# Optimization experiments

Measured on AMD Instinct MI355X. Metric: run time of the kernel, lower is better.

## Reference

```python
import jax, jax.numpy as jnp
import numpy as np

B, N, D_IN, D_OUT = 8, 2048, 256, 256
BN_EPS = 1e-5
SELU_ALPHA = 1.6732632423543772
SELU_SCALE = 1.0507009873554805


def setup_inputs() -> dict:
    key = jax.random.key(0)
    k1, k2, k3, k4 = jax.random.split(key, 4)
    lim_lin = 1.0 / np.sqrt(D_IN)
    return {
        "x": jax.random.normal(k1, (B, N, D_IN), dtype=jnp.float32),
        "w_map": jax.random.uniform(k2, (D_IN,), jnp.float32, -lim_lin, lim_lin),
        "w_att": jax.random.uniform(k3, (D_OUT, D_IN), jnp.float32, -lim_lin, lim_lin),
        "w_res": jax.random.uniform(k4, (D_OUT, D_IN), jnp.float32, -lim_lin, lim_lin),
        "gamma": jnp.ones((D_OUT,), jnp.float32),
        "beta": jnp.zeros((D_OUT,), jnp.float32),
    }


def _selu(x):
    x_clamped = jnp.clip(x, -10.0, 10.0)
    return SELU_SCALE * jnp.where(x > 0, x, SELU_ALPHA * (jnp.exp(x_clamped) - 1.0))


def reference(x, w_map, w_att, w_res, gamma, beta):
    # scores[b,i,j] = sum_d w_map[d] * x[b,i,d] * x[b,j,d]  (== W_map(x_i*x_j))
    scores = jnp.einsum("bid,bjd->bij", x * w_map, x)  # [B,N,N]
    attn = jax.nn.softmax(scores, axis=-1)
    aggregated = jnp.einsum("bij,bjd->bid", attn, x)  # [B,N,D]
    out = aggregated @ w_att.T + x @ w_res.T  # [B,N,D_OUT]
    # BatchNorm1d in training mode: stats over (batch, nodes) per channel, biased var
    mean = jnp.mean(out, axis=(0, 1))
    var = jnp.mean(jnp.square(out - mean), axis=(0, 1))
    out = (out - mean) * jax.lax.rsqrt(var + BN_EPS) * gamma + beta
    return _selu(out)
```

## Files before the change

### kernel.cpp

```cpp
#include <hip/hip_runtime.h>
#include <hip/hip_bf16.h>


typedef __attribute__((ext_vector_type(8)))  short bf16x8;
typedef __attribute__((ext_vector_type(4)))  float f32x4;
typedef __attribute__((ext_vector_type(16))) float f32x16;

#define MFMA16(a, b, c) __builtin_amdgcn_mfma_f32_16x16x32_bf16((a), (b), (c), 0, 0, 0)
#define MFMA32(a, b, c) __builtin_amdgcn_mfma_f32_32x32x16_bf16((a), (b), (c), 0, 0, 0)

constexpr int   NB = 8, NN = 2048;
constexpr int   ROWS = NB * NN;
constexpr float BN_EPS = 1e-5f;
constexpr float SELU_ALPHA = 1.6732632423543772f;
constexpr float SELU_SCALE = 1.0507009873554805f;

__device__ __forceinline__ unsigned short f2bf(float f) {
  union { float f; unsigned int u; } v; v.f = f;
  unsigned int u = v.u;
  u += 0x7FFFu + ((u >> 16) & 1u);
  return (unsigned short)(u >> 16);
}
__device__ __forceinline__ float bf2f(unsigned short h) {
  union { float f; unsigned int u; } v; v.u = ((unsigned int)h) << 16;
  return v.f;
}
__device__ __forceinline__ unsigned int pk2(float lo, float hi) {
  return (unsigned int)f2bf(lo) | ((unsigned int)f2bf(hi) << 16);
}

__device__ __forceinline__ void async_copy16(const unsigned short* g, unsigned short* l) {
  __builtin_amdgcn_global_load_lds(
      (const __attribute__((address_space(1))) void*)g,
      (__attribute__((address_space(3))) void*)l, 16, 0, 0);
}

__global__ __launch_bounds__(256) void k0_prep(const float* __restrict__ x,
                                               unsigned short* __restrict__ XR,
                                               unsigned short* __restrict__ Xt,
                                               const float* __restrict__ w_att,
                                               const float* __restrict__ w_res,
                                               unsigned short* __restrict__ WC,
                                               float* __restrict__ sums) {
  __shared__ unsigned short Ls[32 * 264];
  const int t = threadIdx.x;
  const int b = blockIdx.x & 7, rt = blockIdx.x >> 3;
  const int grb = b * NN + rt * 32;
  const int c = (t & 31) * 8, r0 = t >> 5;
#pragma unroll
  for (int q = 0; q < 4; ++q) {
    int r = r0 + q * 8;
    const float* xp = x + (size_t)(grb + r) * 256 + c;
    float4 a = *(const float4*)xp;
    float4 d = *(const float4*)(xp + 4);
    union { unsigned short s[8]; uint4 v; } xb;
    xb.s[0] = f2bf(a.x); xb.s[1] = f2bf(a.y); xb.s[2] = f2bf(a.z); xb.s[3] = f2bf(a.w);
    xb.s[4] = f2bf(d.x); xb.s[5] = f2bf(d.y); xb.s[6] = f2bf(d.z); xb.s[7] = f2bf(d.w);
    *(uint4*)(XR + (size_t)(grb + r) * 256 + c) = xb.v;
    *(uint4*)&Ls[r * 264 + c] = xb.v;
  }
  __syncthreads();
  unsigned short* dstB = Xt + (size_t)b * 256 * 2048 + rt * 32;
  const int dl = t >> 2, jc = t & 3;
#pragma unroll
  for (int pass = 0; pass < 4; ++pass) {
    int d = pass * 64 + dl;
    union { unsigned short s[8]; uint4 v; } o;
#pragma unroll
    for (int j = 0; j < 8; ++j) o.s[j] = Ls[(jc * 8 + j) * 264 + d];
    *(uint4*)(dstB + (size_t)d * 2048 + jc * 8) = o.v;
  }
  if (blockIdx.x == 0 && t < 256) ((float4*)sums)[t] = make_float4(0.f, 0.f, 0.f, 0.f);
  if (blockIdx.x < 64) {
    int f = (blockIdx.x * 256 + t) * 8;
    int cc = f >> 9, k = f & 511;
    const float* src = (k < 256) ? (w_att + cc * 256 + k) : (w_res + cc * 256 + (k - 256));
    float4 a = *(const float4*)src;
    float4 d = *(const float4*)(src + 4);
    union { unsigned short s[8]; uint4 v; } o;
    o.s[0] = f2bf(a.x); o.s[1] = f2bf(a.y); o.s[2] = f2bf(a.z); o.s[3] = f2bf(a.w);
    o.s[4] = f2bf(d.x); o.s[5] = f2bf(d.y); o.s[6] = f2bf(d.z); o.s[7] = f2bf(d.w);
    *(uint4*)(WC + f) = o.v;
  }
}

__global__ __launch_bounds__(512, 2) void k1_attn(const float* __restrict__ w_map,
                                                  const unsigned short* __restrict__ XR,
                                                  const unsigned short* __restrict__ Xt,
                                                  unsigned short* __restrict__ Opart,
                                                  float* __restrict__ Lpart) {
  __shared__ unsigned short Ks[2][32 * 256];
  __shared__ unsigned short Vt[2][256 * 32];

  const int t = threadIdx.x;
  const int w = t >> 6, lane = t & 63;
  const int l31 = lane & 31, h = lane >> 5;
  const int qb = blockIdx.x >> 2, p = blockIdx.x & 3;
  const int b = qb >> 3;
  const int rowbase = qb * 256;
  const int jb0 = b * 2048 + p * 512;
  const unsigned short* Xtb = Xt + (size_t)b * 256 * 2048;

  int kSrc[2], vSrc[2];
#pragma unroll
  for (int q = 0; q < 2; ++q) {
    int cch = q * 512 + t;
    int kj = cch >> 5, kck = cch & 31;
    int pj = ((kj >> 3) & 1) * 16 + ((kj >> 4) & 1) * 4 + (kj & 3) + ((kj >> 2) & 1) * 8;
    kSrc[q] = (jb0 + pj) * 256 + ((kck ^ (kj & 7)) * 8);
    int vd = cch >> 2, vcj = cch & 3;
    vSrc[q] = vd * 2048 + p * 512 + ((vcj ^ ((vd >> 1) & 3)) * 8);
  }

#pragma unroll
  for (int q = 0; q < 2; ++q)
    async_copy16(XR + kSrc[q], &Ks[0][(q * 512 + t) * 8]);
#pragma unroll
  for (int q = 0; q < 2; ++q)
    async_copy16(Xtb + vSrc[q], &Vt[0][(q * 512 + t) * 8]);

  bf16x8 qf[16];
  {
    const unsigned short* xrow = XR + (size_t)(rowbase + w * 32 + l31) * 256 + h * 8;
#pragma unroll
    for (int kc = 0; kc < 16; ++kc) {
      bf16x8 xb = *(const bf16x8*)(xrow + kc * 16);
      const float* wp = w_map + kc * 16 + h * 8;
      float4 w0 = *(const float4*)wp, w1 = *(const float4*)(wp + 4);
      float wv[8] = {w0.x, w0.y, w0.z, w0.w, w1.x, w1.y, w1.z, w1.w};
      bf16x8 qv;
#pragma unroll
      for (int i = 0; i < 8; ++i)
        qv[i] = (short)f2bf(bf2f((unsigned short)xb[i]) * wv[i]);
      qf[kc] = qv;
    }
  }

  const f32x16 fz16 = {0.f,0.f,0.f,0.f, 0.f,0.f,0.f,0.f, 0.f,0.f,0.f,0.f, 0.f,0.f,0.f,0.f};
  f32x16 oacc[8];
#pragma unroll
  for (int i = 0; i < 8; ++i) oacc[i] = fz16;
  float rsum = 0.f;

  const int sw7 = l31 & 7;
  const int vkey = (l31 >> 1) & 3;

  for (int jt = 0; jt < 16; ++jt) {
    const int cur = jt & 1;
    __syncthreads();
    if (jt < 15) {
#pragma unroll
      for (int q = 0; q < 2; ++q)
        async_copy16(XR + kSrc[q] + (jt + 1) * 8192, &Ks[cur ^ 1][(q * 512 + t) * 8]);
#pragma unroll
      for (int q = 0; q < 2; ++q)
        async_copy16(Xtb + vSrc[q] + (jt + 1) * 32, &Vt[cur ^ 1][(q * 512 + t) * 8]);
    }
    f32x16 sA = fz16, sB = fz16;
#pragma unroll
    for (int kc = 0; kc < 8; ++kc) {
      bf16x8 kf = *(const bf16x8*)&Ks[cur][l31 * 256 + (((2 * kc + h) ^ sw7) * 8)];
      sA = MFMA32(kf, qf[kc], sA);
    }
#pragma unroll
    for (int kc = 8; kc < 16; ++kc) {
      bf16x8 kf = *(const bf16x8*)&Ks[cur][l31 * 256 + (((2 * kc + h) ^ sw7) * 8)];
      sB = MFMA32(kf, qf[kc], sB);
    }
    float pv[16];
#pragma unroll
    for (int r = 0; r < 16; ++r) {
      pv[r] = __expf(sA[r] + sB[r]);
      rsum += pv[r];
    }
    union { unsigned int u[4]; bf16x8 v; } a0, a1;
    a0.u[0] = pk2(pv[0],  pv[1]);
    a0.u[1] = pk2(pv[2],  pv[3]);
    a0.u[2] = pk2(pv[8],  pv[9]);
    a0.u[3] = pk2(pv[10], pv[11]);
    a1.u[0] = pk2(pv[4],  pv[5]);
    a1.u[1] = pk2(pv[6],  pv[7]);
    a1.u[2] = pk2(pv[12], pv[13]);
    a1.u[3] = pk2(pv[14], pv[15]);
#pragma unroll
    for (int dt = 0; dt < 8; ++dt) {
      const int dbase = (dt * 32 + l31) * 32;
      bf16x8 v0 = *(const bf16x8*)&Vt[cur][dbase + ((h ^ vkey) * 8)];
      oacc[dt] = MFMA32(a0.v, v0, oacc[dt]);
      bf16x8 v1 = *(const bf16x8*)&Vt[cur][dbase + (((2 + h) ^ vkey) * 8)];
      oacc[dt] = MFMA32(a1.v, v1, oacc[dt]);
    }
  }

  float rsT = rsum + __shfl_xor(rsum, 32);
  if (h == 0) Lpart[(size_t)p * ROWS + rowbase + w * 32 + l31] = rsT;
  unsigned short* ob = Opart + ((size_t)p * ROWS + rowbase + w * 32) * 256 + l31;
#pragma unroll
  for (int dt = 0; dt < 8; ++dt)
#pragma unroll
    for (int r = 0; r < 16; ++r) {
      int qrow = (r & 3) + ((r >> 2) << 3) + (h << 2);
      ob[qrow * 256 + dt * 32] = f2bf(oacc[dt][r]);
    }
}

__global__ __launch_bounds__(256) void kc_comb(const unsigned short* __restrict__ Opart,
                                               const float* __restrict__ Lpart,
                                               unsigned short* __restrict__ Oagg) {
  const int t = threadIdx.x;
  const int row = blockIdx.x * 8 + (t >> 5);
  const int col = (t & 31) * 8;
  const float invL = 1.0f / (Lpart[row] + Lpart[ROWS + row] +
                             Lpart[2 * ROWS + row] + Lpart[3 * ROWS + row]);
  const size_t base = (size_t)row * 256 + col;
  union { unsigned short s[8]; uint4 v; } p0, p1, p2, p3, o;
  p0.v = *(const uint4*)(Opart + base);
  p1.v = *(const uint4*)(Opart + (size_t)ROWS * 256 + base);
  p2.v = *(const uint4*)(Opart + (size_t)2 * ROWS * 256 + base);
  p3.v = *(const uint4*)(Opart + (size_t)3 * ROWS * 256 + base);
#pragma unroll
  for (int e = 0; e < 8; ++e)
    o.s[e] = f2bf(((bf2f(p0.s[e]) + bf2f(p1.s[e])) + (bf2f(p2.s[e]) + bf2f(p3.s[e]))) * invL);
  *(uint4*)(Oagg + base) = o.v;
}

__global__ __launch_bounds__(256, 2) void k2_gemm(const unsigned short* __restrict__ XR,
                                                  const unsigned short* __restrict__ Oagg,
                                                  const unsigned short* __restrict__ WC,
                                                  float* __restrict__ out,
                                                  float* __restrict__ sums) {
  __shared__ unsigned short As[128 * 72];
  __shared__ unsigned short Bs[64 * 72];
  __shared__ float cs[64], cq[64];
  const int t = threadIdx.x;
  const int w = t >> 6, lane = t & 63, l15 = lane & 15, quad = lane >> 4;
  const int m0 = (blockIdx.x >> 2) * 128, n0 = (blockIdx.x & 3) * 64;
  if (t < 64) { cs[t] = 0.f; cq[t] = 0.f; }

  const f32x4 fz = {0.f, 0.f, 0.f, 0.f};
  f32x4 acc[4][2];
#pragma unroll
  for (int i = 0; i < 4; ++i) { acc[i][0] = fz; acc[i][1] = fz; }

  for (int kk = 0; kk < 512; kk += 64) {
    __syncthreads();
#pragma unroll
    for (int q = 0; q < 4; ++q) {
      int idx = t + q * 256;
      int row = idx >> 3, koff = (idx & 7) * 8;
      const unsigned short* src = (kk < 256)
          ? (Oagg + (size_t)(m0 + row) * 256 + kk + koff)
          : (XR + (size_t)(m0 + row) * 256 + (kk - 256) + koff);
      *(uint4*)&As[row * 72 + koff] = *(const uint4*)src;
    }
#pragma unroll
    for (int q = 0; q < 2; ++q) {
      int idx = t + q * 256;
      int row = idx >> 3, koff = (idx & 7) * 8;
      *(uint4*)&Bs[row * 72 + koff] = *(const uint4*)(WC + (size_t)(n0 + row) * 512 + kk + koff);
    }
    __syncthreads();
#pragma unroll
    for (int kc = 0; kc < 2; ++kc) {
      bf16x8 b0 = *(const bf16x8*)&Bs[((w >> 1) * 32 + l15) * 72 + kc * 32 + quad * 8];
      bf16x8 b1 = *(const bf16x8*)&Bs[((w >> 1) * 32 + 16 + l15) * 72 + kc * 32 + quad * 8];
#pragma unroll
      for (int mt = 0; mt < 4; ++mt) {
        bf16x8 af = *(const bf16x8*)&As[((w & 1) * 64 + mt * 16 + l15) * 72 + kc * 32 + quad * 8];
        acc[mt][0] = MFMA16(af, b0, acc[mt][0]);
        acc[mt][1] = MFMA16(af, b1, acc[mt][1]);
      }
    }
  }
#pragma unroll
  for (int mt = 0; mt < 4; ++mt)
#pragma unroll
    for (int nt = 0; nt < 2; ++nt)
#pragma unroll
      for (int r = 0; r < 4; ++r) {
        int grow = m0 + (w & 1) * 64 + mt * 16 + quad * 4 + r;
        int gcol = n0 + (w >> 1) * 32 + nt * 16 + l15;
        out[(size_t)grow * 256 + gcol] = acc[mt][nt][r];
      }
#pragma unroll
  for (int nt = 0; nt < 2; ++nt) {
    float a = 0.f, b2 = 0.f;
#pragma unroll
    for (int mt = 0; mt < 4; ++mt)
#pragma unroll
      for (int r = 0; r < 4; ++r) {
        float v = acc[mt][nt][r];
        a += v; b2 += v * v;
      }
    a += __shfl_xor(a, 16);  a += __shfl_xor(a, 32);
    b2 += __shfl_xor(b2, 16); b2 += __shfl_xor(b2, 32);
    if (quad == 0) {
      int ci = (w >> 1) * 32 + nt * 16 + l15;
      atomicAdd(&cs[ci], a);
      atomicAdd(&cq[ci], b2);
    }
  }
  __syncthreads();
  if (t < 64) {
    atomicAdd(&sums[n0 + t], cs[t]);
    atomicAdd(&sums[256 + n0 + t], cq[t]);
  }
}

__global__ __launch_bounds__(256) void k4_bn_selu(float* __restrict__ out,
                                                  const float* __restrict__ sums,
                                                  const float* __restrict__ gamma,
                                                  const float* __restrict__ beta) {
  int f = (blockIdx.x * 256 + threadIdx.x) * 8;
  int c = f & 255;
  const float inv_m = 1.0f / 16384.0f;
  float4 v0 = *(const float4*)(out + f);
  float4 v1 = *(const float4*)(out + f + 4);
  float vv[8] = {v0.x, v0.y, v0.z, v0.w, v1.x, v1.y, v1.z, v1.w};
#pragma unroll
  for (int k = 0; k < 8; ++k) {
    int ch = c + k;
    float mean = sums[ch] * inv_m;
    float var = sums[256 + ch] * inv_m - mean * mean;
    float y = (vv[k] - mean) * rsqrtf(var + BN_EPS) * gamma[ch] + beta[ch];
    float yc = fminf(fmaxf(y, -10.f), 10.f);
    float r = (y > 0.f) ? y : (SELU_ALPHA * (expf(yc) - 1.0f));
    vv[k] = SELU_SCALE * r;
  }
  float4 o0 = {vv[0], vv[1], vv[2], vv[3]};
  float4 o1 = {vv[4], vv[5], vv[6], vv[7]};
  *(float4*)(out + f) = o0;
  *(float4*)(out + f + 4) = o1;
}

extern "C" void kernel_launch(void* const* d_in, const int* in_sizes, int n_in,
                              void* d_out, int out_size, void* d_ws, size_t ws_size,
                              hipStream_t stream) {
  const float* x     = (const float*)d_in[0];
  const float* w_map = (const float*)d_in[1];
  const float* w_att = (const float*)d_in[2];
  const float* w_res = (const float*)d_in[3];
  const float* gamma = (const float*)d_in[4];
  const float* beta  = (const float*)d_in[5];
  float* out = (float*)d_out;

  unsigned short* XR = (unsigned short*)d_ws;
  unsigned short* Xt = XR + (size_t)ROWS * 256;
  unsigned short* WC = Xt + (size_t)NB * 256 * 2048;
  unsigned short* Opart = WC + 256 * 512;
  float* Lpart = (float*)(Opart + (size_t)4 * ROWS * 256);
  float* sums  = Lpart + 4 * ROWS;
  unsigned short* Oagg = Xt;

  k0_prep<<<512, 256, 0, stream>>>(x, XR, Xt, w_att, w_res, WC, sums);
  k1_attn<<<256, 512, 0, stream>>>(w_map, XR, Xt, Opart, Lpart);
  kc_comb<<<2048, 256, 0, stream>>>(Opart, Lpart, Oagg);
  k2_gemm<<<512, 256, 0, stream>>>(XR, Oagg, WC, out, sums);
  k4_bn_selu<<<2048, 256, 0, stream>>>(out, sums, gamma, beta);
}
```

Baseline: 160.6 us.

## Fuse split-K partial combine into output GEMM with full-width N tiles

Removes the separate combine kernel by reducing the four attention partial outputs and normalizing by the summed softmax denominators while loading A tiles inside the GEMM. The GEMM is retiled to 32 rows by all 256 output columns per 512-thread block, so each A tile is loaded and combined once instead of once per column block. This saves a launch and the write/read of the combined intermediate. In exchange each block loads the full weight matrix per K step, and only half the threads load A.

```diff
diff --git a/kernel.cpp b/kernel.cpp
--- a/kernel.cpp
+++ b/kernel.cpp
@@ -204,89 +204,86 @@
     }
 }
 
-__global__ __launch_bounds__(256) void kc_comb(const unsigned short* __restrict__ Opart,
-                                               const float* __restrict__ Lpart,
-                                               unsigned short* __restrict__ Oagg) {
-  const int t = threadIdx.x;
-  const int row = blockIdx.x * 8 + (t >> 5);
-  const int col = (t & 31) * 8;
-  const float invL = 1.0f / (Lpart[row] + Lpart[ROWS + row] +
-                             Lpart[2 * ROWS + row] + Lpart[3 * ROWS + row]);
-  const size_t base = (size_t)row * 256 + col;
-  union { unsigned short s[8]; uint4 v; } p0, p1, p2, p3, o;
-  p0.v = *(const uint4*)(Opart + base);
-  p1.v = *(const uint4*)(Opart + (size_t)ROWS * 256 + base);
-  p2.v = *(const uint4*)(Opart + (size_t)2 * ROWS * 256 + base);
-  p3.v = *(const uint4*)(Opart + (size_t)3 * ROWS * 256 + base);
-#pragma unroll
-  for (int e = 0; e < 8; ++e)
-    o.s[e] = f2bf(((bf2f(p0.s[e]) + bf2f(p1.s[e])) + (bf2f(p2.s[e]) + bf2f(p3.s[e]))) * invL);
-  *(uint4*)(Oagg + base) = o.v;
-}
-
-__global__ __launch_bounds__(256, 2) void k2_gemm(const unsigned short* __restrict__ XR,
-                                                  const unsigned short* __restrict__ Oagg,
+__global__ __launch_bounds__(512, 2) void k2_gemm(const unsigned short* __restrict__ XR,
+                                                  const unsigned short* __restrict__ Opart,
+                                                  const float* __restrict__ Lpart,
                                                   const unsigned short* __restrict__ WC,
                                                   float* __restrict__ out,
                                                   float* __restrict__ sums) {
-  __shared__ unsigned short As[128 * 72];
-  __shared__ unsigned short Bs[64 * 72];
-  __shared__ float cs[64], cq[64];
+  __shared__ unsigned short As[32 * 72];
+  __shared__ unsigned short Bs[256 * 72];
+  __shared__ float cs[256], cq[256];
+  __shared__ float invLs[32];
   const int t = threadIdx.x;
   const int w = t >> 6, lane = t & 63, l15 = lane & 15, quad = lane >> 4;
-  const int m0 = (blockIdx.x >> 2) * 128, n0 = (blockIdx.x & 3) * 64;
-  if (t < 64) { cs[t] = 0.f; cq[t] = 0.f; }
+  const int m0 = blockIdx.x * 32;
+  if (t < 32) {
+    int row = m0 + t;
+    invLs[t] = 1.0f / (Lpart[row] + Lpart[ROWS + row] +
+                       Lpart[2 * ROWS + row] + Lpart[3 * ROWS + row]);
+  }
 
   const f32x4 fz = {0.f, 0.f, 0.f, 0.f};
-  f32x4 acc[4][2];
-#pragma unroll
-  for (int i = 0; i < 4; ++i) { acc[i][0] = fz; acc[i][1] = fz; }
+  f32x4 acc[2][2];
+#pragma unroll
+  for (int i = 0; i < 2; ++i) { acc[i][0] = fz; acc[i][1] = fz; }
 
   for (int kk = 0; kk < 512; kk += 64) {
     __syncthreads();
-#pragma unroll
-    for (int q = 0; q < 4; ++q) {
-      int idx = t + q * 256;
+    if (t < 256) {
+      int row = t >> 3, koff = (t & 7) * 8;
+      if (kk < 256) {
+        size_t base = (size_t)(m0 + row) * 256 + kk + koff;
+        union { unsigned short s[8]; uint4 v; } p0, p1, p2, p3, o;
+        p0.v = *(const uint4*)(Opart + base);
+        p1.v = *(const uint4*)(Opart + (size_t)ROWS * 256 + base);
+        p2.v = *(const uint4*)(Opart + (size_t)2 * ROWS * 256 + base);
+        p3.v = *(const uint4*)(Opart + (size_t)3 * ROWS * 256 + base);
+        float il = invLs[row];
+#pragma unroll
+        for (int e = 0; e < 8; ++e)
+          o.s[e] = f2bf(((bf2f(p0.s[e]) + bf2f(p1.s[e])) +
+                         (bf2f(p2.s[e]) + bf2f(p3.s[e]))) * il);
+        *(uint4*)&As[row * 72 + koff] = o.v;
+      } else {
+        *(uint4*)&As[row * 72 + koff] =
+            *(const uint4*)(XR + (size_t)(m0 + row) * 256 + (kk - 256) + koff);
+      }
+    }
+#pragma unroll
+    for (int i = 0; i < 4; ++i) {
+      int idx = t + i * 512;
       int row = idx >> 3, koff = (idx & 7) * 8;
-      const unsigned short* src = (kk < 256)
-          ? (Oagg + (size_t)(m0 + row) * 256 + kk + koff)
-          : (XR + (size_t)(m0 + row) * 256 + (kk - 256) + koff);
-      *(uint4*)&As[row * 72 + koff] = *(const uint4*)src;
-    }
-#pragma unroll
-    for (int q = 0; q < 2; ++q) {
-      int idx = t + q * 256;
-      int row = idx >> 3, koff = (idx & 7) * 8;
-      *(uint4*)&Bs[row * 72 + koff] = *(const uint4*)(WC + (size_t)(n0 + row) * 512 + kk + koff);
+      *(uint4*)&Bs[row * 72 + koff] = *(const uint4*)(WC + (size_t)row * 512 + kk + koff);
     }
     __syncthreads();
 #pragma unroll
     for (int kc = 0; kc < 2; ++kc) {
-      bf16x8 b0 = *(const bf16x8*)&Bs[((w >> 1) * 32 + l15) * 72 + kc * 32 + quad * 8];
-      bf16x8 b1 = *(const bf16x8*)&Bs[((w >> 1) * 32 + 16 + l15) * 72 + kc * 32 + quad * 8];
-#pragma unroll
-      for (int mt = 0; mt < 4; ++mt) {
-        bf16x8 af = *(const bf16x8*)&As[((w & 1) * 64 + mt * 16 + l15) * 72 + kc * 32 + quad * 8];
-        acc[mt][0] = MFMA16(af, b0, acc[mt][0]);
-        acc[mt][1] = MFMA16(af, b1, acc[mt][1]);
+      bf16x8 a0 = *(const bf16x8*)&As[l15 * 72 + kc * 32 + quad * 8];
+      bf16x8 a1 = *(const bf16x8*)&As[(16 + l15) * 72 + kc * 32 + quad * 8];
+#pragma unroll
+      for (int nt = 0; nt < 2; ++nt) {
+        bf16x8 bf = *(const bf16x8*)&Bs[(w * 32 + nt * 16 + l15) * 72 + kc * 32 + quad * 8];
+        acc[0][nt] = MFMA16(a0, bf, acc[0][nt]);
+        acc[1][nt] = MFMA16(a1, bf, acc[1][nt]);
       }
     }
   }
 #pragma unroll
-  for (int mt = 0; mt < 4; ++mt)
+  for (int mt = 0; mt < 2; ++mt)
 #pragma unroll
     for (int nt = 0; nt < 2; ++nt)
 #pragma unroll
       for (int r = 0; r < 4; ++r) {
-        int grow = m0 + (w & 1) * 64 + mt * 16 + quad * 4 + r;
-        int gcol = n0 + (w >> 1) * 32 + nt * 16 + l15;
+        int grow = m0 + mt * 16 + quad * 4 + r;
+        int gcol = w * 32 + nt * 16 + l15;
         out[(size_t)grow * 256 + gcol] = acc[mt][nt][r];
       }
 #pragma unroll
   for (int nt = 0; nt < 2; ++nt) {
     float a = 0.f, b2 = 0.f;
 #pragma unroll
-    for (int mt = 0; mt < 4; ++mt)
+    for (int mt = 0; mt < 2; ++mt)
 #pragma unroll
       for (int r = 0; r < 4; ++r) {
         float v = acc[mt][nt][r];
@@ -295,15 +292,15 @@
     a += __shfl_xor(a, 16);  a += __shfl_xor(a, 32);
     b2 += __shfl_xor(b2, 16); b2 += __shfl_xor(b2, 32);
     if (quad == 0) {
-      int ci = (w >> 1) * 32 + nt * 16 + l15;
-      atomicAdd(&cs[ci], a);
-      atomicAdd(&cq[ci], b2);
+      int ci = w * 32 + nt * 16 + l15;
+      cs[ci] = a;
+      cq[ci] = b2;
     }
   }
   __syncthreads();
-  if (t < 64) {
-    atomicAdd(&sums[n0 + t], cs[t]);
-    atomicAdd(&sums[256 + n0 + t], cq[t]);
+  if (t < 256) {
+    atomicAdd(&sums[t], cs[t]);
+    atomicAdd(&sums[256 + t], cq[t]);
   }
 }
 
@@ -350,11 +347,9 @@
   unsigned short* Opart = WC + 256 * 512;
   float* Lpart = (float*)(Opart + (size_t)4 * ROWS * 256);
   float* sums  = Lpart + 4 * ROWS;
-  unsigned short* Oagg = Xt;
 
   k0_prep<<<512, 256, 0, stream>>>(x, XR, Xt, w_att, w_res, WC, sums);
   k1_attn<<<256, 512, 0, stream>>>(w_map, XR, Xt, Opart, Lpart);
-  kc_comb<<<2048, 256, 0, stream>>>(Opart, Lpart, Oagg);
-  k2_gemm<<<512, 256, 0, stream>>>(XR, Oagg, WC, out, sums);
+  k2_gemm<<<512, 512, 0, stream>>>(XR, Opart, Lpart, WC, out, sums);
   k4_bn_selu<<<2048, 256, 0, stream>>>(out, sums, gamma, beta);
 }
```

Result: slower. 165.3 us (+2.9%).
